# Kernel optimization log

Measured on AMD Instinct MI355X. Metric: run time of the kernel, lower is better.

Reference implementation:

```python
import jax, jax.numpy as jnp
import numpy as np

N, IN, HID, OUT = 500_000, 16, 128, 1
E = 1_000_000


def setup_inputs() -> dict:
    key = jax.random.key(0)
    ks = jax.random.split(key, 32)
    f32 = jnp.float32

    def nrm(k, shape, scale=0.05):
        return jax.random.normal(k, shape, dtype=f32) * scale

    inp = {
        "x": jax.random.normal(ks[0], (N, IN), dtype=f32),
        "edge_index": jax.random.randint(ks[1], (2, E), 0, N),
        "edge_weight": jax.random.uniform(ks[2], (E,), dtype=f32),
        # GCLSTM input->gate weights W_* : [IN, HID]
        "W_i": nrm(ks[3], (IN, HID)), "W_f": nrm(ks[4], (IN, HID)),
        "W_c": nrm(ks[5], (IN, HID)), "W_o": nrm(ks[6], (IN, HID)),
        # ChebConv(K=1) per gate: single Linear(HID,HID) weight + conv bias
        "Uc_i": nrm(ks[7], (HID, HID)), "Uc_f": nrm(ks[8], (HID, HID)),
        "Uc_c": nrm(ks[9], (HID, HID)), "Uc_o": nrm(ks[10], (HID, HID)),
        "bc_i": jnp.zeros((HID,), f32), "bc_f": jnp.zeros((HID,), f32),
        "bc_c": jnp.zeros((HID,), f32), "bc_o": jnp.zeros((HID,), f32),
        # peephole weights w_c_* : [1, HID]
        "w_ci": nrm(ks[11], (1, HID)), "w_cf": nrm(ks[12], (1, HID)),
        "w_co": nrm(ks[13], (1, HID)),
        # gate biases b_* : [1, HID]
        "b_i": jnp.zeros((1, HID), f32), "b_f": jnp.zeros((1, HID), f32),
        "b_c": jnp.zeros((1, HID), f32), "b_o": jnp.zeros((1, HID), f32),
        # MLP head: HID -> HID//2 -> HID//4 -> OUT
        "M1": nrm(ks[14], (HID, HID // 2)), "bm1": jnp.zeros((HID // 2,), f32),
        "M2": nrm(ks[15], (HID // 2, HID // 4)), "bm2": jnp.zeros((HID // 4,), f32),
        "M3": nrm(ks[16], (HID // 4, OUT)), "bm3": jnp.zeros((OUT,), f32),
    }
    return inp


def reference(x, edge_index, edge_weight, W_i, W_f, W_c, W_o,
              Uc_i, Uc_f, Uc_c, Uc_o, bc_i, bc_f, bc_c, bc_o,
              w_ci, w_cf, w_co, b_i, b_f, b_c, b_o,
              M1, bm1, M2, bm2, M3, bm3):
    x = x.astype(jnp.float32)
    n, hid = x.shape[0], W_i.shape[1]
    # GCLSTM single step; H, C default-initialized to zeros.
    H = jnp.zeros((n, hid), x.dtype)
    C = jnp.zeros((n, hid), x.dtype)

    # ChebConv with K=1: out = lins[0](T_0(L) H) + bias = H @ U + b
    # (no neighbor propagation term; edge_index/edge_weight unused).
    def cheb(Hm, U, b):
        return Hm @ U + b

    I = jax.nn.sigmoid(x @ W_i + cheb(H, Uc_i, bc_i) + w_ci * C + b_i)
    Fg = jax.nn.sigmoid(x @ W_f + cheb(H, Uc_f, bc_f) + w_cf * C + b_f)
    T = jnp.tanh(x @ W_c + cheb(H, Uc_c, bc_c) + b_c)
    C = Fg * C + I * T
    O = jax.nn.sigmoid(x @ W_o + cheb(H, Uc_o, bc_o) + w_co * C + b_o)
    H = O * jnp.tanh(C)

    h = jax.nn.relu(H)
    h = jax.nn.relu(h @ M1 + bm1)
    h = jax.nn.relu(h @ M2 + bm2)
    out = h @ M3 + bm3            # [N, 1]
    return out.squeeze(-1)        # [N]  (original has typo .sequeeze; intent is squeeze)
```

## Files before the change

kernel.cpp:

```cpp
#include <hip/hip_runtime.h>
#include <stdint.h>


typedef __attribute__((ext_vector_type(8))) short bf16x8;
typedef __attribute__((ext_vector_type(4))) float f32x4;

constexpr int IN_F = 16;
constexpr int HID  = 128;
constexpr int MH1  = 64;
constexpr int MH2  = 32;
constexpr int WAVES = 8;
constexpr int ITER  = 2;
constexpr int TILES_PER_BLOCK = WAVES * ITER;

constexpr float LOG2E = 1.4426950408889634f;
constexpr float TWO_L = 2.8853900817779268f;

constexpr int GATE_F = 0;
constexpr int M1_F   = 12288;
constexpr int M2_F   = 28672;
constexpr int BIAS_O = 32768;
constexpr int WCO_O  = 34304;
constexpr int M3_O   = 34816;
constexpr int BM1_O  = 34944;
constexpr int BM2_O  = 35200;
constexpr int BM3_O  = 35328;
constexpr int SCR_O  = 35840;
constexpr int LDS_BYTES = SCR_O + WAVES * 4096;

__device__ __forceinline__ short f2bf(float f) {
    uint32_t u = __builtin_bit_cast(uint32_t, f);
    u += 0x7fffu + ((u >> 16) & 1u);
    return (short)(u >> 16);
}
__device__ __forceinline__ uint32_t cvt_pk(float lo, float hi) {
    uint32_t r;
    asm("v_cvt_pk_bf16_f32 %0, %1, %2" : "=v"(r) : "v"(lo), "v"(hi));
    return r;
}

__global__ __launch_bounds__(512) void gclstm_mfma_kernel(
    const float* __restrict__ x,
    const float* __restrict__ W_i, const float* __restrict__ W_c, const float* __restrict__ W_o,
    const float* __restrict__ bc_i, const float* __restrict__ bc_c, const float* __restrict__ bc_o,
    const float* __restrict__ w_co,
    const float* __restrict__ b_i, const float* __restrict__ b_c, const float* __restrict__ b_o,
    const float* __restrict__ M1, const float* __restrict__ bm1,
    const float* __restrict__ M2, const float* __restrict__ bm2,
    const float* __restrict__ M3, const float* __restrict__ bm3,
    float* __restrict__ out, int n)
{
    __shared__ char lds[LDS_BYTES];
    const int tid  = threadIdx.x;
    const int wid  = tid >> 6;
    const int lane = tid & 63;
    const int g    = lane >> 4;
    const int ln   = lane & 15;

    if (lane < 32) {
        for (int t = wid; t < 24; t += WAVES) {
            const int gi = t >> 3, mt = t & 7;
            const float* Wg = (gi == 0) ? W_i : (gi == 1) ? W_c : W_o;
            const float sc  = (gi == 1) ? TWO_L : -LOG2E;
            const int row = mt * 16 + ln;
            const int k0  = g * 8;
            bf16x8 v;
            #pragma unroll
            for (int j = 0; j < 8; ++j) v[j] = f2bf(Wg[(k0 + j) * HID + row] * sc);
            *(bf16x8*)(lds + GATE_F + t * 512 + lane * 16) = v;
        }
    }
    for (int t = wid; t < 16; t += WAVES) {
        const int mt = t >> 2, kt = t & 3;
        const int row = mt * 16 + ln;
        const int k0  = kt * 32 + g * 8;
        bf16x8 v;
        #pragma unroll
        for (int j = 0; j < 8; ++j) v[j] = f2bf(M1[(k0 + j) * MH1 + row]);
        *(bf16x8*)(lds + M1_F + t * 1024 + lane * 16) = v;
    }
    for (int t = wid; t < 4; t += WAVES) {
        const int mt = t >> 1, kt = t & 1;
        const int row = mt * 16 + ln;
        const int k0  = kt * 32 + g * 8;
        bf16x8 v;
        #pragma unroll
        for (int j = 0; j < 8; ++j) v[j] = f2bf(M2[(k0 + j) * MH2 + row]);
        *(bf16x8*)(lds + M2_F + t * 1024 + lane * 16) = v;
    }
    {
        float* biasS = (float*)(lds + BIAS_O);
        if (tid < HID) {
            biasS[tid]           = (bc_i[tid] + b_i[tid]) * (-LOG2E);
            biasS[HID + tid]     = (bc_c[tid] + b_c[tid]) * TWO_L;
            biasS[2 * HID + tid] = (bc_o[tid] + b_o[tid]) * (-LOG2E);
            ((float*)(lds + WCO_O))[tid] = -0.5f * w_co[tid];
        }
        if (tid < MH1) ((float*)(lds + BM1_O))[tid] = bm1[tid];
        if (tid < MH2) { ((float*)(lds + M3_O))[tid]  = M3[tid];
                         ((float*)(lds + BM2_O))[tid] = bm2[tid]; }
        if (tid == 0)  ((float*)(lds + BM3_O))[0] = bm3[0];
    }
    __syncthreads();

    char* HT  = lds + SCR_O + wid * 4096;
    char* M1T = HT;
    const float* biasI = (const float*)(lds + BIAS_O);
    const float* biasC = biasI + HID;
    const float* biasO = biasC + HID;
    const float* wcoS  = (const float*)(lds + WCO_O);
    const float* m3S   = (const float*)(lds + M3_O);
    const float* bm1S  = (const float*)(lds + BM1_O);
    const float* bm2S  = (const float*)(lds + BM2_O);
    const float  bm3v  = ((const float*)(lds + BM3_O))[0];

    for (int it = 0; it < ITER; ++it) {
        const long tileIdx = (long)blockIdx.x * TILES_PER_BLOCK + it * WAVES + wid;
        const long base = tileIdx * 16;
        if (base >= n) break;

        bf16x8 xf;
        #pragma unroll
        for (int j = 0; j < 8; ++j) xf[j] = 0;
        if (g < 2) {
            const float* xp = x + (base + ln) * IN_F + g * 8;
            float4 a = *(const float4*)xp;
            float4 b = *(const float4*)(xp + 4);
            union { uint32_t u[4]; bf16x8 v; } cv;
            cv.u[0] = cvt_pk(a.x, a.y); cv.u[1] = cvt_pk(a.z, a.w);
            cv.u[2] = cvt_pk(b.x, b.y); cv.u[3] = cvt_pk(b.z, b.w);
            xf = cv.v;
        }

        #pragma unroll
        for (int mt = 0; mt < 8; ++mt) {
            const int h0 = mt * 16 + g * 4;
            bf16x8 fi = *(const bf16x8*)(lds + GATE_F + (0 * 8 + mt) * 512 + (lane & 31) * 16);
            bf16x8 fc = *(const bf16x8*)(lds + GATE_F + (1 * 8 + mt) * 512 + (lane & 31) * 16);
            bf16x8 fo = *(const bf16x8*)(lds + GATE_F + (2 * 8 + mt) * 512 + (lane & 31) * 16);
            f32x4 bI = *(const f32x4*)(biasI + h0);
            f32x4 bC = *(const f32x4*)(biasC + h0);
            f32x4 bO = *(const f32x4*)(biasO + h0);
            f32x4 ai = __builtin_amdgcn_mfma_f32_16x16x32_bf16(fi, xf, bI, 0, 0, 0);
            f32x4 ac = __builtin_amdgcn_mfma_f32_16x16x32_bf16(fc, xf, bC, 0, 0, 0);
            f32x4 ao = __builtin_amdgcn_mfma_f32_16x16x32_bf16(fo, xf, bO, 0, 0, 0);

            f32x4 wc = *(const f32x4*)(wcoS + h0);
            float hv[4];
            #pragma unroll
            for (int i = 0; i < 4; ++i) {
                float Ei = __builtin_amdgcn_exp2f(ai[i]);
                float Ec = __builtin_amdgcn_exp2f(ac[i]);
                float R1 = __builtin_amdgcn_rcpf((1.0f + Ei) * (1.0f + Ec));
                float cp = (Ec - 1.0f) * R1 * TWO_L;
                float Eo = __builtin_amdgcn_exp2f(fmaf(wc[i], cp, ao[i]));
                float E2 = __builtin_amdgcn_exp2f(cp);
                float R2 = __builtin_amdgcn_rcpf((1.0f + Eo) * (E2 + 1.0f));
                hv[i] = fmaxf((E2 - 1.0f) * R2, 0.0f);
            }
            char* dst = HT + (mt >> 1) * 1024
                          + ((((mt & 1) * 2 + (g >> 1)) * 16 + ln) * 16)
                          + (g & 1) * 8;
            uint2 hp; hp.x = cvt_pk(hv[0], hv[1]); hp.y = cvt_pk(hv[2], hv[3]);
            *(uint2*)dst = hp;
        }

        bf16x8 hb0 = *(const bf16x8*)(HT + 0 * 1024 + lane * 16);
        bf16x8 hb1 = *(const bf16x8*)(HT + 1 * 1024 + lane * 16);
        bf16x8 hb2 = *(const bf16x8*)(HT + 2 * 1024 + lane * 16);
        bf16x8 hb3 = *(const bf16x8*)(HT + 3 * 1024 + lane * 16);
        #pragma unroll
        for (int mt = 0; mt < 4; ++mt) {
            const int r0 = mt * 16 + g * 4;
            f32x4 acc = *(const f32x4*)(bm1S + r0);
            acc = __builtin_amdgcn_mfma_f32_16x16x32_bf16(
                *(const bf16x8*)(lds + M1_F + (mt * 4 + 0) * 1024 + lane * 16), hb0, acc, 0, 0, 0);
            acc = __builtin_amdgcn_mfma_f32_16x16x32_bf16(
                *(const bf16x8*)(lds + M1_F + (mt * 4 + 1) * 1024 + lane * 16), hb1, acc, 0, 0, 0);
            acc = __builtin_amdgcn_mfma_f32_16x16x32_bf16(
                *(const bf16x8*)(lds + M1_F + (mt * 4 + 2) * 1024 + lane * 16), hb2, acc, 0, 0, 0);
            acc = __builtin_amdgcn_mfma_f32_16x16x32_bf16(
                *(const bf16x8*)(lds + M1_F + (mt * 4 + 3) * 1024 + lane * 16), hb3, acc, 0, 0, 0);
            float mv[4];
            #pragma unroll
            for (int i = 0; i < 4; ++i) mv[i] = fmaxf(acc[i], 0.f);
            char* dst = M1T + (mt >> 1) * 1024
                            + ((((mt & 1) * 2 + (g >> 1)) * 16 + ln) * 16)
                            + (g & 1) * 8;
            uint2 mp; mp.x = cvt_pk(mv[0], mv[1]); mp.y = cvt_pk(mv[2], mv[3]);
            *(uint2*)dst = mp;
        }

        bf16x8 mb0 = *(const bf16x8*)(M1T + 0 * 1024 + lane * 16);
        bf16x8 mb1 = *(const bf16x8*)(M1T + 1 * 1024 + lane * 16);
        float outacc = 0.f;
        #pragma unroll
        for (int mt = 0; mt < 2; ++mt) {
            const int r0 = mt * 16 + g * 4;
            f32x4 acc = *(const f32x4*)(bm2S + r0);
            acc = __builtin_amdgcn_mfma_f32_16x16x32_bf16(
                *(const bf16x8*)(lds + M2_F + (mt * 2 + 0) * 1024 + lane * 16), mb0, acc, 0, 0, 0);
            acc = __builtin_amdgcn_mfma_f32_16x16x32_bf16(
                *(const bf16x8*)(lds + M2_F + (mt * 2 + 1) * 1024 + lane * 16), mb1, acc, 0, 0, 0);
            f32x4 w3 = *(const f32x4*)(m3S + r0);
            #pragma unroll
            for (int i = 0; i < 4; ++i)
                outacc = fmaf(fmaxf(acc[i], 0.f), w3[i], outacc);
        }
        outacc += __shfl_xor(outacc, 16);
        outacc += __shfl_xor(outacc, 32);
        if (lane < 16) out[base + lane] = outacc + bm3v;
    }
}

extern "C" void kernel_launch(void* const* d_in, const int* in_sizes, int n_in,
                              void* d_out, int out_size, void* d_ws, size_t ws_size,
                              hipStream_t stream) {
    const float* x    = (const float*)d_in[0];
    const float* W_i  = (const float*)d_in[3];
    const float* W_c  = (const float*)d_in[5];
    const float* W_o  = (const float*)d_in[6];
    const float* bc_i = (const float*)d_in[11];
    const float* bc_c = (const float*)d_in[13];
    const float* bc_o = (const float*)d_in[14];
    const float* w_co = (const float*)d_in[17];
    const float* b_i  = (const float*)d_in[18];
    const float* b_c  = (const float*)d_in[20];
    const float* b_o  = (const float*)d_in[21];
    const float* M1   = (const float*)d_in[22];
    const float* bm1  = (const float*)d_in[23];
    const float* M2   = (const float*)d_in[24];
    const float* bm2  = (const float*)d_in[25];
    const float* M3   = (const float*)d_in[26];
    const float* bm3  = (const float*)d_in[27];
    float* out = (float*)d_out;

    const int n = in_sizes[0] / IN_F;
    const int tiles = (n + 15) / 16;
    const int grid = (tiles + TILES_PER_BLOCK - 1) / TILES_PER_BLOCK;

    gclstm_mfma_kernel<<<grid, 512, 0, stream>>>(
        x, W_i, W_c, W_o, bc_i, bc_c, bc_o, w_co,
        b_i, b_c, b_o, M1, bm1, M2, bm2, M3, bm3, out, n);
}
```

Baseline: 69.85 us.

## Keep MFMA outputs in registers by permuting weight rows, dropping LDS scratch

The hidden-unit order of the gate weights, biases and M1 rows is permuted. Each lane's MFMA accumulator outputs then line up directly with the B-operand layout the next MFMA stage needs. This removes the per-wave LDS scratch round trip (store, then reload) for H and the M1 activations, which shrinks LDS use. A launch-bounds occupancy hint is also added. The cost is a trickier index mapping that must stay consistent across every stage, plus more register pressure from holding the packed activations.

```diff
diff --git a/kernel.cpp b/kernel.cpp
--- a/kernel.cpp
+++ b/kernel.cpp
@@ -25,8 +25,7 @@
 constexpr int BM1_O  = 34944;
 constexpr int BM2_O  = 35200;
 constexpr int BM3_O  = 35328;
-constexpr int SCR_O  = 35840;
-constexpr int LDS_BYTES = SCR_O + WAVES * 4096;
+constexpr int LDS_BYTES = 35392;
 
 __device__ __forceinline__ short f2bf(float f) {
     uint32_t u = __builtin_bit_cast(uint32_t, f);
@@ -38,8 +37,11 @@
     asm("v_cvt_pk_bf16_f32 %0, %1, %2" : "=v"(r) : "v"(lo), "v"(hi));
     return r;
 }
-
-__global__ __launch_bounds__(512) void gclstm_mfma_kernel(
+__device__ __forceinline__ int permrow(int mt, int r) {
+    return ((mt >> 1) << 5) + ((r >> 2) << 3) + ((mt & 1) << 2) + (r & 3);
+}
+
+__global__ __launch_bounds__(512, 8) void gclstm_mfma_kernel(
     const float* __restrict__ x,
     const float* __restrict__ W_i, const float* __restrict__ W_c, const float* __restrict__ W_o,
     const float* __restrict__ bc_i, const float* __restrict__ bc_c, const float* __restrict__ bc_o,
@@ -50,7 +52,7 @@
     const float* __restrict__ M3, const float* __restrict__ bm3,
     float* __restrict__ out, int n)
 {
-    __shared__ char lds[LDS_BYTES];
+    __shared__ __align__(16) char lds[LDS_BYTES];
     const int tid  = threadIdx.x;
     const int wid  = tid >> 6;
     const int lane = tid & 63;
@@ -62,7 +64,7 @@
             const int gi = t >> 3, mt = t & 7;
             const float* Wg = (gi == 0) ? W_i : (gi == 1) ? W_c : W_o;
             const float sc  = (gi == 1) ? TWO_L : -LOG2E;
-            const int row = mt * 16 + ln;
+            const int row = permrow(mt, ln);
             const int k0  = g * 8;
             bf16x8 v;
             #pragma unroll
@@ -72,7 +74,7 @@
     }
     for (int t = wid; t < 16; t += WAVES) {
         const int mt = t >> 2, kt = t & 3;
-        const int row = mt * 16 + ln;
+        const int row = permrow(mt, ln);
         const int k0  = kt * 32 + g * 8;
         bf16x8 v;
         #pragma unroll
@@ -91,20 +93,22 @@
     {
         float* biasS = (float*)(lds + BIAS_O);
         if (tid < HID) {
-            biasS[tid]           = (bc_i[tid] + b_i[tid]) * (-LOG2E);
-            biasS[HID + tid]     = (bc_c[tid] + b_c[tid]) * TWO_L;
-            biasS[2 * HID + tid] = (bc_o[tid] + b_o[tid]) * (-LOG2E);
-            ((float*)(lds + WCO_O))[tid] = -0.5f * w_co[tid];
-        }
-        if (tid < MH1) ((float*)(lds + BM1_O))[tid] = bm1[tid];
+            const int h = permrow(tid >> 4, tid & 15);
+            biasS[tid]           = (bc_i[h] + b_i[h]) * (-LOG2E);
+            biasS[HID + tid]     = (bc_c[h] + b_c[h]) * TWO_L;
+            biasS[2 * HID + tid] = (bc_o[h] + b_o[h]) * (-LOG2E);
+            ((float*)(lds + WCO_O))[tid] = -0.5f * w_co[h];
+        }
+        if (tid < MH1) {
+            const int m = permrow(tid >> 4, tid & 15);
+            ((float*)(lds + BM1_O))[tid] = bm1[m];
+        }
         if (tid < MH2) { ((float*)(lds + M3_O))[tid]  = M3[tid];
                          ((float*)(lds + BM2_O))[tid] = bm2[tid]; }
         if (tid == 0)  ((float*)(lds + BM3_O))[0] = bm3[0];
     }
     __syncthreads();
 
-    char* HT  = lds + SCR_O + wid * 4096;
-    char* M1T = HT;
     const float* biasI = (const float*)(lds + BIAS_O);
     const float* biasC = biasI + HID;
     const float* biasO = biasC + HID;
@@ -132,6 +136,7 @@
             xf = cv.v;
         }
 
+        uint32_t hpk[16];
         #pragma unroll
         for (int mt = 0; mt < 8; ++mt) {
             const int h0 = mt * 16 + g * 4;
@@ -158,50 +163,43 @@
                 float R2 = __builtin_amdgcn_rcpf((1.0f + Eo) * (E2 + 1.0f));
                 hv[i] = fmaxf((E2 - 1.0f) * R2, 0.0f);
             }
-            char* dst = HT + (mt >> 1) * 1024
-                          + ((((mt & 1) * 2 + (g >> 1)) * 16 + ln) * 16)
-                          + (g & 1) * 8;
-            uint2 hp; hp.x = cvt_pk(hv[0], hv[1]); hp.y = cvt_pk(hv[2], hv[3]);
-            *(uint2*)dst = hp;
-        }
-
-        bf16x8 hb0 = *(const bf16x8*)(HT + 0 * 1024 + lane * 16);
-        bf16x8 hb1 = *(const bf16x8*)(HT + 1 * 1024 + lane * 16);
-        bf16x8 hb2 = *(const bf16x8*)(HT + 2 * 1024 + lane * 16);
-        bf16x8 hb3 = *(const bf16x8*)(HT + 3 * 1024 + lane * 16);
+            hpk[mt * 2]     = cvt_pk(hv[0], hv[1]);
+            hpk[mt * 2 + 1] = cvt_pk(hv[2], hv[3]);
+        }
+
+        uint32_t mpk[8];
         #pragma unroll
         for (int mt = 0; mt < 4; ++mt) {
             const int r0 = mt * 16 + g * 4;
             f32x4 acc = *(const f32x4*)(bm1S + r0);
-            acc = __builtin_amdgcn_mfma_f32_16x16x32_bf16(
-                *(const bf16x8*)(lds + M1_F + (mt * 4 + 0) * 1024 + lane * 16), hb0, acc, 0, 0, 0);
-            acc = __builtin_amdgcn_mfma_f32_16x16x32_bf16(
-                *(const bf16x8*)(lds + M1_F + (mt * 4 + 1) * 1024 + lane * 16), hb1, acc, 0, 0, 0);
-            acc = __builtin_amdgcn_mfma_f32_16x16x32_bf16(
-                *(const bf16x8*)(lds + M1_F + (mt * 4 + 2) * 1024 + lane * 16), hb2, acc, 0, 0, 0);
-            acc = __builtin_amdgcn_mfma_f32_16x16x32_bf16(
-                *(const bf16x8*)(lds + M1_F + (mt * 4 + 3) * 1024 + lane * 16), hb3, acc, 0, 0, 0);
+            #pragma unroll
+            for (int kt = 0; kt < 4; ++kt) {
+                union { uint32_t u[4]; bf16x8 v; } b;
+                b.u[0] = hpk[4 * kt + 0]; b.u[1] = hpk[4 * kt + 1];
+                b.u[2] = hpk[4 * kt + 2]; b.u[3] = hpk[4 * kt + 3];
+                acc = __builtin_amdgcn_mfma_f32_16x16x32_bf16(
+                    *(const bf16x8*)(lds + M1_F + (mt * 4 + kt) * 1024 + lane * 16), b.v, acc, 0, 0, 0);
+            }
             float mv[4];
             #pragma unroll
             for (int i = 0; i < 4; ++i) mv[i] = fmaxf(acc[i], 0.f);
-            char* dst = M1T + (mt >> 1) * 1024
-                            + ((((mt & 1) * 2 + (g >> 1)) * 16 + ln) * 16)
-                            + (g & 1) * 8;
-            uint2 mp; mp.x = cvt_pk(mv[0], mv[1]); mp.y = cvt_pk(mv[2], mv[3]);
-            *(uint2*)dst = mp;
-        }
-
-        bf16x8 mb0 = *(const bf16x8*)(M1T + 0 * 1024 + lane * 16);
-        bf16x8 mb1 = *(const bf16x8*)(M1T + 1 * 1024 + lane * 16);
+            mpk[mt * 2]     = cvt_pk(mv[0], mv[1]);
+            mpk[mt * 2 + 1] = cvt_pk(mv[2], mv[3]);
+        }
+
         float outacc = 0.f;
         #pragma unroll
         for (int mt = 0; mt < 2; ++mt) {
             const int r0 = mt * 16 + g * 4;
             f32x4 acc = *(const f32x4*)(bm2S + r0);
-            acc = __builtin_amdgcn_mfma_f32_16x16x32_bf16(
-                *(const bf16x8*)(lds + M2_F + (mt * 2 + 0) * 1024 + lane * 16), mb0, acc, 0, 0, 0);
-            acc = __builtin_amdgcn_mfma_f32_16x16x32_bf16(
-                *(const bf16x8*)(lds + M2_F + (mt * 2 + 1) * 1024 + lane * 16), mb1, acc, 0, 0, 0);
+            #pragma unroll
+            for (int kt = 0; kt < 2; ++kt) {
+                union { uint32_t u[4]; bf16x8 v; } b;
+                b.u[0] = mpk[4 * kt + 0]; b.u[1] = mpk[4 * kt + 1];
+                b.u[2] = mpk[4 * kt + 2]; b.u[3] = mpk[4 * kt + 3];
+                acc = __builtin_amdgcn_mfma_f32_16x16x32_bf16(
+                    *(const bf16x8*)(lds + M2_F + (mt * 2 + kt) * 1024 + lane * 16), b.v, acc, 0, 0, 0);
+            }
             f32x4 w3 = *(const f32x4*)(m3S + r0);
             #pragma unroll
             for (int i = 0; i < 4; ++i)
```

After: 62.07 us. -11.1%, faster.
